# Kernel tuning notes

Hardware: AMD Instinct MI355X
Metric: run time of the kernel (lower is better)

## Reference

```python
import jax, jax.numpy as jnp
import numpy as np

def setup_inputs() -> dict:
    key = jax.random.key(0)
    x = jax.random.normal(key, (8, 4096, 4096), dtype=jnp.float32)
    return {"x": x}

def reference(x):
    # Inclusive prefix sum over the last axis, identical math to the
    # torch unbind/add/stack loop.
    return jnp.cumsum(x, axis=-1)
```

## Files before the change

kernel.cpp:

```cpp
#include <hip/hip_runtime.h>

#define ROW_LEN 4096
#define BLOCK 256
#define PER_THREAD 16

__global__ __launch_bounds__(BLOCK) void row_cumsum_kernel(
    const float* __restrict__ in, float* __restrict__ out) {
    const size_t row = blockIdx.x;
    const float* src = in + row * (size_t)ROW_LEN;
    float* dst = out + row * (size_t)ROW_LEN;
    const int t = threadIdx.x;

    const float4* s4 = reinterpret_cast<const float4*>(src + t * PER_THREAD);
    float4 a = s4[0];
    float4 b = s4[1];
    float4 c = s4[2];
    float4 d = s4[3];

    float v[PER_THREAD];
    v[0]  = a.x; v[1]  = a.y; v[2]  = a.z; v[3]  = a.w;
    v[4]  = b.x; v[5]  = b.y; v[6]  = b.z; v[7]  = b.w;
    v[8]  = c.x; v[9]  = c.y; v[10] = c.z; v[11] = c.w;
    v[12] = d.x; v[13] = d.y; v[14] = d.z; v[15] = d.w;

    #pragma unroll
    for (int i = 1; i < PER_THREAD; ++i) v[i] += v[i - 1];
    const float total = v[PER_THREAD - 1];

    const int lane = t & 63;
    const int wave = t >> 6;
    float x = total;
    #pragma unroll
    for (int off = 1; off < 64; off <<= 1) {
        float y = __shfl_up(x, off, 64);
        if (lane >= off) x += y;
    }

    __shared__ float wsum[BLOCK / 64];
    if (lane == 63) wsum[wave] = x;
    __syncthreads();
    float wexcl = 0.0f;
    #pragma unroll
    for (int w = 0; w < BLOCK / 64; ++w) {
        if (w < wave) wexcl += wsum[w];
    }

    const float excl = wexcl + (x - total);
    #pragma unroll
    for (int i = 0; i < PER_THREAD; ++i) v[i] += excl;

    float4* d4 = reinterpret_cast<float4*>(dst + t * PER_THREAD);
    d4[0] = make_float4(v[0],  v[1],  v[2],  v[3]);
    d4[1] = make_float4(v[4],  v[5],  v[6],  v[7]);
    d4[2] = make_float4(v[8],  v[9],  v[10], v[11]);
    d4[3] = make_float4(v[12], v[13], v[14], v[15]);
}

extern "C" void kernel_launch(void* const* d_in, const int* in_sizes, int n_in,
                              void* d_out, int out_size, void* d_ws, size_t ws_size,
                              hipStream_t stream) {
    const float* x = (const float*)d_in[0];
    float* out = (float*)d_out;
    const int n_rows = in_sizes[0] / ROW_LEN;
    row_cumsum_kernel<<<n_rows, BLOCK, 0, stream>>>(x, out);
}
```

Before: 197.5 us.

## Use coalesced segmented layout with per-segment wave scans for row cumsum

```diff
diff --git a/kernel.cpp b/kernel.cpp
--- a/kernel.cpp
+++ b/kernel.cpp
@@ -2,7 +2,9 @@
 
 #define ROW_LEN 4096
 #define BLOCK 256
-#define PER_THREAD 16
+#define SEGS 4
+#define SEG_LEN 1024
+#define NWAVES 4
 
 __global__ __launch_bounds__(BLOCK) void row_cumsum_kernel(
     const float* __restrict__ in, float* __restrict__ out) {
@@ -10,50 +12,57 @@
     const float* src = in + row * (size_t)ROW_LEN;
     float* dst = out + row * (size_t)ROW_LEN;
     const int t = threadIdx.x;
+    const int lane = t & 63;
+    const int wave = t >> 6;
 
-    const float4* s4 = reinterpret_cast<const float4*>(src + t * PER_THREAD);
-    float4 a = s4[0];
-    float4 b = s4[1];
-    float4 c = s4[2];
-    float4 d = s4[3];
+    float4 seg[SEGS];
+    #pragma unroll
+    for (int s = 0; s < SEGS; ++s)
+        seg[s] = reinterpret_cast<const float4*>(src + s * SEG_LEN)[t];
 
-    float v[PER_THREAD];
-    v[0]  = a.x; v[1]  = a.y; v[2]  = a.z; v[3]  = a.w;
-    v[4]  = b.x; v[5]  = b.y; v[6]  = b.z; v[7]  = b.w;
-    v[8]  = c.x; v[9]  = c.y; v[10] = c.z; v[11] = c.w;
-    v[12] = d.x; v[13] = d.y; v[14] = d.z; v[15] = d.w;
+    float tot[SEGS], x[SEGS];
+    #pragma unroll
+    for (int s = 0; s < SEGS; ++s) {
+        seg[s].y += seg[s].x;
+        seg[s].z += seg[s].y;
+        seg[s].w += seg[s].z;
+        tot[s] = seg[s].w;
+        x[s] = tot[s];
+        #pragma unroll
+        for (int off = 1; off < 64; off <<= 1) {
+            float y = __shfl_up(x[s], off, 64);
+            if (lane >= off) x[s] += y;
+        }
+    }
+
+    __shared__ float wsum[SEGS][NWAVES];
+    if (lane == 63) {
+        #pragma unroll
+        for (int s = 0; s < SEGS; ++s) wsum[s][wave] = x[s];
+    }
+    __syncthreads();
+
+    float prevseg = 0.0f;
+    #pragma unroll
+    for (int s = 0; s < SEGS; ++s) {
+        float waveexcl = 0.0f, segtot = 0.0f;
+        #pragma unroll
+        for (int w = 0; w < NWAVES; ++w) {
+            float v = wsum[s][w];
+            segtot += v;
+            if (w < wave) waveexcl += v;
+        }
+        const float excl = prevseg + waveexcl + (x[s] - tot[s]);
+        seg[s].x += excl;
+        seg[s].y += excl;
+        seg[s].z += excl;
+        seg[s].w += excl;
+        prevseg += segtot;
+    }
 
     #pragma unroll
-    for (int i = 1; i < PER_THREAD; ++i) v[i] += v[i - 1];
-    const float total = v[PER_THREAD - 1];
-
-    const int lane = t & 63;
-    const int wave = t >> 6;
-    float x = total;
-    #pragma unroll
-    for (int off = 1; off < 64; off <<= 1) {
-        float y = __shfl_up(x, off, 64);
-        if (lane >= off) x += y;
-    }
-
-    __shared__ float wsum[BLOCK / 64];
-    if (lane == 63) wsum[wave] = x;
-    __syncthreads();
-    float wexcl = 0.0f;
-    #pragma unroll
-    for (int w = 0; w < BLOCK / 64; ++w) {
-        if (w < wave) wexcl += wsum[w];
-    }
-
-    const float excl = wexcl + (x - total);
-    #pragma unroll
-    for (int i = 0; i < PER_THREAD; ++i) v[i] += excl;
-
-    float4* d4 = reinterpret_cast<float4*>(dst + t * PER_THREAD);
-    d4[0] = make_float4(v[0],  v[1],  v[2],  v[3]);
-    d4[1] = make_float4(v[4],  v[5],  v[6],  v[7]);
-    d4[2] = make_float4(v[8],  v[9],  v[10], v[11]);
-    d4[3] = make_float4(v[12], v[13], v[14], v[15]);
+    for (int s = 0; s < SEGS; ++s)
+        reinterpret_cast<float4*>(dst + s * SEG_LEN)[t] = seg[s];
 }
 
 extern "C" void kernel_launch(void* const* d_in, const int* in_sizes, int n_in,
```

Result: no change. 193.7 us (-1.9%).
